# Performance work log

Hardware: AMD Instinct MI355X
Metric: run time of the kernel (lower is better)

The kernel has to match this reference:

```python
import jax, jax.numpy as jnp
import numpy as np
import math

DIM = 1024
HEADS = 16
HEAD_DIM = DIM // HEADS
FFN = 4096
B, S = 2, 2048
EPS = 1e-12


def layernorm(x, w, b):
    u = jnp.mean(x, axis=-1, keepdims=True)
    s = jnp.mean((x - u) ** 2, axis=-1, keepdims=True)
    return w * ((x - u) / jnp.sqrt(s + EPS)) + b


def setup_inputs() -> dict:
    key = jax.random.key(0)
    ks = jax.random.split(key, 8)
    scale = 0.02
    return {
        "x": jax.random.normal(ks[0], (B, S, DIM), dtype=jnp.float32),
        "mask": jnp.zeros((1, 1, S, S), dtype=jnp.float32),
        "wq": jax.random.normal(ks[1], (DIM, DIM), dtype=jnp.float32) * scale,
        "wk": jax.random.normal(ks[2], (DIM, DIM), dtype=jnp.float32) * scale,
        "wv": jax.random.normal(ks[3], (DIM, DIM), dtype=jnp.float32) * scale,
        "wo": jax.random.normal(ks[4], (DIM, DIM), dtype=jnp.float32) * scale,
        "w1": jax.random.normal(ks[5], (DIM, FFN), dtype=jnp.float32) * scale,
        "w2": jax.random.normal(ks[6], (FFN, DIM), dtype=jnp.float32) * scale,
        "ln1_w": jnp.ones((DIM,), dtype=jnp.float32),
        "ln1_b": jnp.zeros((DIM,), dtype=jnp.float32),
        "ln2_w": jnp.ones((DIM,), dtype=jnp.float32),
        "ln2_b": jnp.zeros((DIM,), dtype=jnp.float32),
    }


def reference(x, mask, wq, wk, wv, wo, w1, w2, ln1_w, ln1_b, ln2_w, ln2_b):
    # --- attention sub-block (pre-LN) ---
    h = layernorm(x, ln1_w, ln1_b)
    q = (h @ wq).reshape(B, S, HEADS, HEAD_DIM).transpose(0, 2, 1, 3)  # [B,H,S,D]
    k = (h @ wk).reshape(B, S, HEADS, HEAD_DIM).transpose(0, 2, 1, 3)
    v = (h @ wv).reshape(B, S, HEADS, HEAD_DIM).transpose(0, 2, 1, 3)
    scores = jnp.einsum("bhsd,bhtd->bhst", q, k) / math.sqrt(HEAD_DIM)
    scores = scores + mask
    probs = jax.nn.softmax(scores.astype(jnp.float32), axis=-1).astype(q.dtype)
    attn = jnp.einsum("bhst,bhtd->bhsd", probs, v)  # [B,H,S,D]
    attn = attn.transpose(0, 2, 1, 3).reshape(B, S, DIM)
    x = x + attn @ wo
    # --- FFN sub-block (pre-LN) ---
    h = layernorm(x, ln2_w, ln2_b)
    m = jax.nn.gelu(h @ w1, approximate=False) @ w2
    return x + m
```

## Files before the change

### kernel.cpp

```cpp
#include <hip/hip_runtime.h>
#include <math.h>


#define DIMSZ 1024
#define SEQ   2048
#define BATCH 2
#define NHEAD 16
#define HD    64
#define FFNSZ 4096
#define ROWS  (BATCH*SEQ)

typedef __attribute__((ext_vector_type(8))) short bf8_t;
typedef __attribute__((ext_vector_type(4))) float f4_t;

__device__ __forceinline__ unsigned short f2bf(float f) {
  union { float f; unsigned u; } c; c.f = f;
  unsigned u = c.u;
  return (unsigned short)((u + 0x7fffu + ((u >> 16) & 1u)) >> 16);
}

__device__ __forceinline__ float fast_exp2(float x) {
#if __has_builtin(__builtin_amdgcn_exp2f)
  return __builtin_amdgcn_exp2f(x);
#else
  return exp2f(x);
#endif
}

__device__ __forceinline__ unsigned int pk_trunc_bf16(float a, float b) {
#if __has_builtin(__builtin_amdgcn_perm)
  return __builtin_amdgcn_perm(__float_as_uint(b), __float_as_uint(a), 0x07060302u);
#else
  return (__float_as_uint(b) & 0xffff0000u) | (__float_as_uint(a) >> 16);
#endif
}

__device__ __forceinline__ void async16(const void* g, void* l) {
  __builtin_amdgcn_global_load_lds((const __attribute__((address_space(1))) void*)g,
                                   (__attribute__((address_space(3))) void*)l,
                                   16, 0, 0);
}

__device__ __forceinline__ f4_t mfma_bf16(bf8_t a, bf8_t b, f4_t c) {
  return __builtin_amdgcn_mfma_f32_16x16x32_bf16(a, b, c, 0, 0, 0);
}

__global__ __launch_bounds__(256) void ln_kernel(const float* __restrict__ x,
                                                 const float* __restrict__ w,
                                                 const float* __restrict__ b,
                                                 unsigned short* __restrict__ out) {
  int row  = blockIdx.x * 4 + (threadIdx.x >> 6);
  int lane = threadIdx.x & 63;
  const float4* xr = (const float4*)(x + (size_t)row * DIMSZ);
  float4 v[4];
  float s = 0.f, s2 = 0.f;
#pragma unroll
  for (int i = 0; i < 4; ++i) {
    v[i] = xr[lane + 64*i];
    s  += (v[i].x + v[i].y) + (v[i].z + v[i].w);
    s2 += (v[i].x*v[i].x + v[i].y*v[i].y) + (v[i].z*v[i].z + v[i].w*v[i].w);
  }
#pragma unroll
  for (int off = 32; off; off >>= 1) {
    s  += __shfl_xor(s,  off);
    s2 += __shfl_xor(s2, off);
  }
  float mean = s * (1.f/DIMSZ);
  float var  = s2 * (1.f/DIMSZ) - mean*mean;
  float rstd = rsqrtf(var + 1e-12f);
  const float4* wr = (const float4*)w;
  const float4* br = (const float4*)b;
#pragma unroll
  for (int i = 0; i < 4; ++i) {
    float4 wv = wr[lane + 64*i];
    float4 bv = br[lane + 64*i];
    ushort4 o;
    o.x = f2bf((v[i].x - mean) * rstd * wv.x + bv.x);
    o.y = f2bf((v[i].y - mean) * rstd * wv.y + bv.y);
    o.z = f2bf((v[i].z - mean) * rstd * wv.z + bv.z);
    o.w = f2bf((v[i].w - mean) * rstd * wv.w + bv.w);
    *(ushort4*)(out + (size_t)row * DIMSZ + (size_t)(lane + 64*i) * 4) = o;
  }
}

__global__ __launch_bounds__(256) void wtrans_kernel(const float* __restrict__ w,
                                                     unsigned short* __restrict__ wT,
                                                     int K, int N) {
  __shared__ float t[32][33];
  int tx = threadIdx.x & 31, ty = threadIdx.x >> 5;
  int n0 = blockIdx.x * 32, k0 = blockIdx.y * 32;
#pragma unroll
  for (int i = 0; i < 4; ++i)
    t[ty + 8*i][tx] = w[(size_t)(k0 + ty + 8*i) * N + n0 + tx];
  __syncthreads();
#pragma unroll
  for (int i = 0; i < 4; ++i)
    wT[(size_t)(n0 + ty + 8*i) * K + k0 + tx] = f2bf(t[tx][ty + 8*i]);
}

__global__ __launch_bounds__(256) void vt_kernel(const unsigned short* __restrict__ qkv,
                                                 unsigned short* __restrict__ vt) {
  __shared__ unsigned short tile[64][65];
  int bh = blockIdx.y, b = bh >> 4, h = bh & 15;
  int s0 = blockIdx.x * 64;
  int tx = threadIdx.x & 63, ty = threadIdx.x >> 6;
#pragma unroll
  for (int i = 0; i < 16; ++i) {
    int s = ty + i*4;
    tile[s][tx] = qkv[((size_t)(b*SEQ) + s0 + s) * 3072 + 2048 + h*HD + tx];
  }
  __syncthreads();
#pragma unroll
  for (int i = 0; i < 16; ++i) {
    int d = ty + i*4;
    vt[((size_t)bh * HD + d) * SEQ + s0 + tx] = tile[tx][d];
  }
}

template<int EPI>
__global__ __launch_bounds__(256) void gemm_bt(const unsigned short* __restrict__ A,
                                               const unsigned short* __restrict__ Bt,
                                               void* __restrict__ Cv,
                                               const float* __restrict__ res,
                                               int M, int N, int K) {
  __shared__ unsigned short As[128*32];
  __shared__ unsigned short Bs[128*32];
  int tid  = threadIdx.x;
  int wv   = tid >> 6, lane = tid & 63, quad = lane >> 4, ml = lane & 15;
  int wrow = (wv >> 1) * 64, wcol = (wv & 1) * 64;
  const unsigned short* Ab = A  + (size_t)blockIdx.y * 128 * K;
  const unsigned short* Bb = Bt + (size_t)blockIdx.x * 128 * K;

  f4_t acc[4][4];
#pragma unroll
  for (int i = 0; i < 4; ++i)
#pragma unroll
    for (int j = 0; j < 4; ++j) acc[i][j] = (f4_t){0.f, 0.f, 0.f, 0.f};

  int r0 = tid >> 2, c0 = (tid & 3) * 8;

  for (int k0 = 0; k0 < K; k0 += 32) {
    async16(Ab + (size_t)r0 * K + k0 + c0,        &As[(size_t)tid * 8]);
    async16(Ab + (size_t)(r0+64) * K + k0 + c0,   &As[((size_t)tid + 256) * 8]);
    async16(Bb + (size_t)r0 * K + k0 + c0,        &Bs[(size_t)tid * 8]);
    async16(Bb + (size_t)(r0+64) * K + k0 + c0,   &Bs[((size_t)tid + 256) * 8]);
    __syncthreads();

    bf8_t af[4], bfr[4];
#pragma unroll
    for (int i = 0; i < 4; ++i)
      af[i] = *(const bf8_t*)(&As[(wrow + i*16 + ml) * 32 + quad * 8]);
#pragma unroll
    for (int j = 0; j < 4; ++j)
      bfr[j] = *(const bf8_t*)(&Bs[(wcol + j*16 + ml) * 32 + quad * 8]);
#pragma unroll
    for (int i = 0; i < 4; ++i)
#pragma unroll
      for (int j = 0; j < 4; ++j)
        acc[i][j] = mfma_bf16(af[i], bfr[j], acc[i][j]);
    __syncthreads();
  }

#pragma unroll
  for (int i = 0; i < 4; ++i) {
    int grow = blockIdx.y * 128 + wrow + i*16 + quad*4;
#pragma unroll
    for (int j = 0; j < 4; ++j) {
      int gcol = blockIdx.x * 128 + wcol + j*16 + ml;
#pragma unroll
      for (int r = 0; r < 4; ++r) {
        size_t off = (size_t)(grow + r) * N + gcol;
        float v = acc[i][j][r];
        if constexpr (EPI == 2) {
          ((float*)Cv)[off] = res[off] + v;
        } else {
          if constexpr (EPI == 1)
            v = 0.5f * v * (1.f + erff(v * 0.70710678118654752f));
          ((unsigned short*)Cv)[off] = f2bf(v);
        }
      }
    }
  }
}

__global__ __launch_bounds__(256) void attn_kernel(const unsigned short* __restrict__ qkv,
                                                   const unsigned short* __restrict__ vt,
                                                   const float* __restrict__ mask,
                                                   unsigned short* __restrict__ attnout) {
  __shared__ unsigned short Ks[2][64][32];
  __shared__ unsigned short Vs[2][64][32];
  __shared__ unsigned short Ps[4][16][72];

  int bh = blockIdx.y, b = bh >> 4, h = bh & 15;
  int tid = threadIdx.x;
  int wv = tid >> 6, lane = tid & 63;
  int quad = lane >> 4, ml = lane & 15;
  int q0 = blockIdx.x * 64;
  int q  = q0 + wv * 16 + ml;

  const unsigned short* qrow = qkv + ((size_t)(b*SEQ) + q) * 3072 + h*HD;
  bf8_t qf0 = *(const bf8_t*)(qrow + quad*8);
  bf8_t qf1 = *(const bf8_t*)(qrow + 32 + quad*8);

  const unsigned short* kbase = qkv + (size_t)(b*SEQ) * 3072 + DIMSZ + h*HD;
  const unsigned short* vbase = vt + (size_t)bh * HD * SEQ;
  const float* mrow = mask + (size_t)q * SEQ;

  int srow = tid >> 2;
  int scol = (tid & 3) * 8;

  f4_t O[4];
#pragma unroll
  for (int dt = 0; dt < 4; ++dt) O[dt] = (f4_t){0.f, 0.f, 0.f, 0.f};
  float lR = 0.f;

  const float C1 = 0.18033688011112042f;
  const float C2 = 1.4426950408889634f;

  for (int t0 = 0; t0 < SEQ; t0 += 64) {
    float4 mv[4];
#pragma unroll
    for (int mt = 0; mt < 4; ++mt)
      mv[mt] = *(const float4*)(mrow + t0 + mt*16 + quad*4);

    __syncthreads();
#pragma unroll
    for (int dh = 0; dh < 2; ++dh)
      async16(kbase + (size_t)(t0 + srow) * 3072 + dh*32 + scol,
              &Ks[dh][0][0] + (size_t)tid * 8);
#pragma unroll
    for (int kc = 0; kc < 2; ++kc)
      async16(vbase + (size_t)srow * SEQ + t0 + kc*32 + scol,
              &Vs[kc][0][0] + (size_t)tid * 8);
    __syncthreads();

#pragma unroll
    for (int mt = 0; mt < 4; ++mt) {
      bf8_t kf0 = *(const bf8_t*)(&Ks[0][mt*16 + ml][quad*8]);
      bf8_t kf1 = *(const bf8_t*)(&Ks[1][mt*16 + ml][quad*8]);
      f4_t s = (f4_t){0.f, 0.f, 0.f, 0.f};
      s = mfma_bf16(kf0, qf0, s);
      s = mfma_bf16(kf1, qf1, s);
      float p0 = fast_exp2(fmaf(s[0], C1, mv[mt].x * C2));
      float p1 = fast_exp2(fmaf(s[1], C1, mv[mt].y * C2));
      float p2 = fast_exp2(fmaf(s[2], C1, mv[mt].z * C2));
      float p3 = fast_exp2(fmaf(s[3], C1, mv[mt].w * C2));
      lR += (p0 + p1) + (p2 + p3);
      unsigned int u01 = pk_trunc_bf16(p0, p1);
      unsigned int u23 = pk_trunc_bf16(p2, p3);
      uint2 pk; pk.x = u01; pk.y = u23;
      *(uint2*)(&Ps[wv][ml][mt*16 + quad*4]) = pk;
    }

#pragma unroll
    for (int kc = 0; kc < 2; ++kc) {
      bf8_t pf = *(const bf8_t*)(&Ps[wv][ml][kc*32 + quad*8]);
#pragma unroll
      for (int dt = 0; dt < 4; ++dt) {
        bf8_t vf = *(const bf8_t*)(&Vs[kc][dt*16 + ml][quad*8]);
        O[dt] = mfma_bf16(vf, pf, O[dt]);
      }
    }
  }

  lR += __shfl_xor(lR, 16);
  lR += __shfl_xor(lR, 32);
  float linv = 1.f / lR;
#pragma unroll
  for (int dt = 0; dt < 4; ++dt) {
    ushort4 o;
    o.x = f2bf(O[dt][0] * linv);
    o.y = f2bf(O[dt][1] * linv);
    o.z = f2bf(O[dt][2] * linv);
    o.w = f2bf(O[dt][3] * linv);
    *(ushort4*)(attnout + ((size_t)(b*SEQ) + q) * DIMSZ + h*HD + dt*16 + quad*4) = o;
  }
}

extern "C" void kernel_launch(void* const* d_in, const int* in_sizes, int n_in,
                              void* d_out, int out_size, void* d_ws, size_t ws_size,
                              hipStream_t stream) {
  const float* x    = (const float*)d_in[0];
  const float* mask = (const float*)d_in[1];
  const float* wq   = (const float*)d_in[2];
  const float* wk   = (const float*)d_in[3];
  const float* wvp  = (const float*)d_in[4];
  const float* wo   = (const float*)d_in[5];
  const float* w1   = (const float*)d_in[6];
  const float* w2   = (const float*)d_in[7];
  const float* ln1w = (const float*)d_in[8];
  const float* ln1b = (const float*)d_in[9];
  const float* ln2w = (const float*)d_in[10];
  const float* ln2b = (const float*)d_in[11];
  float* out = (float*)d_out;

  char* ws = (char*)d_ws;
  unsigned short* wqkvT  = (unsigned short*)(ws + 0);
  unsigned short* woT    = (unsigned short*)(ws + 6291456);
  unsigned short* w1T    = (unsigned short*)(ws + 8388608);
  unsigned short* w2T    = (unsigned short*)(ws + 16777216);
  unsigned short* attno  = (unsigned short*)(ws + 25165824);
  float*          x2     = (float*)         (ws + 33554432);
  unsigned short* hbuf   = (unsigned short*)(ws + 50331648);
  unsigned short* qkvb   = (unsigned short*)(ws + 58720256);
  unsigned short* vtb    = (unsigned short*)(ws + 83886080);
  unsigned short* gbuf   = (unsigned short*)(ws + 58720256);

  ln_kernel<<<ROWS/4, 256, 0, stream>>>(x, ln1w, ln1b, hbuf);
  wtrans_kernel<<<dim3(32, 32),  256, 0, stream>>>(wq,  wqkvT,                 1024, 1024);
  wtrans_kernel<<<dim3(32, 32),  256, 0, stream>>>(wk,  wqkvT + 1024*1024,     1024, 1024);
  wtrans_kernel<<<dim3(32, 32),  256, 0, stream>>>(wvp, wqkvT + 2*1024*1024,   1024, 1024);
  wtrans_kernel<<<dim3(32, 32),  256, 0, stream>>>(wo,  woT,                   1024, 1024);
  wtrans_kernel<<<dim3(128, 32), 256, 0, stream>>>(w1,  w1T,                   1024, 4096);
  wtrans_kernel<<<dim3(32, 128), 256, 0, stream>>>(w2,  w2T,                   4096, 1024);
  gemm_bt<0><<<dim3(3072/128, 4096/128), 256, 0, stream>>>(hbuf, wqkvT, qkvb, nullptr, ROWS, 3072, 1024);
  vt_kernel<<<dim3(SEQ/64, BATCH*NHEAD), 256, 0, stream>>>(qkvb, vtb);
  attn_kernel<<<dim3(SEQ/64, BATCH*NHEAD), 256, 0, stream>>>(qkvb, vtb, mask, attno);
  gemm_bt<2><<<dim3(1024/128, 4096/128), 256, 0, stream>>>(attno, woT, x2, x, ROWS, 1024, 1024);
  ln_kernel<<<ROWS/4, 256, 0, stream>>>(x2, ln2w, ln2b, hbuf);
  gemm_bt<1><<<dim3(4096/128, 4096/128), 256, 0, stream>>>(hbuf, w1T, gbuf, nullptr, ROWS, FFNSZ, 1024);
  gemm_bt<2><<<dim3(1024/128, 4096/128), 256, 0, stream>>>(gbuf, w2T, out, x2, ROWS, 1024, 4096);

  (void)in_sizes; (void)n_in; (void)out_size; (void)ws_size;
}
```

Baseline: 475.8 us.

## Double-buffer K/V tiles in attention and merge square weight transposes

The attention kernel now keeps two LDS buffers for K and V tiles and prefetches the next 64-key tile (plus its mask values) while computing the current one, removing the load-then-compute serialization per iteration. The four 1024x1024 weight transposes are merged into one launch using blockIdx.z to select the matrix, reducing launch count. This doubles the K/V shared memory per block and increases register use for the extra mask vectors, which could reduce occupancy.

After: 477.6 us. About the same (+0.4%).

```diff
diff --git a/kernel.cpp b/kernel.cpp
--- a/kernel.cpp
+++ b/kernel.cpp
@@ -81,6 +81,29 @@
     o.w = f2bf((v[i].w - mean) * rstd * wv.w + bv.w);
     *(ushort4*)(out + (size_t)row * DIMSZ + (size_t)(lane + 64*i) * 4) = o;
   }
+}
+
+__global__ __launch_bounds__(256) void wtrans4_kernel(const float* __restrict__ w0,
+                                                      const float* __restrict__ w1,
+                                                      const float* __restrict__ w2,
+                                                      const float* __restrict__ w3,
+                                                      unsigned short* __restrict__ o0,
+                                                      unsigned short* __restrict__ o1,
+                                                      unsigned short* __restrict__ o2,
+                                                      unsigned short* __restrict__ o3) {
+  const int K = 1024, N = 1024;
+  const float* w = (blockIdx.z == 0) ? w0 : (blockIdx.z == 1) ? w1 : (blockIdx.z == 2) ? w2 : w3;
+  unsigned short* wT = (blockIdx.z == 0) ? o0 : (blockIdx.z == 1) ? o1 : (blockIdx.z == 2) ? o2 : o3;
+  __shared__ float t[32][33];
+  int tx = threadIdx.x & 31, ty = threadIdx.x >> 5;
+  int n0 = blockIdx.x * 32, k0 = blockIdx.y * 32;
+#pragma unroll
+  for (int i = 0; i < 4; ++i)
+    t[ty + 8*i][tx] = w[(size_t)(k0 + ty + 8*i) * N + n0 + tx];
+  __syncthreads();
+#pragma unroll
+  for (int i = 0; i < 4; ++i)
+    wT[(size_t)(n0 + ty + 8*i) * K + k0 + tx] = f2bf(t[tx][ty + 8*i]);
 }
 
 __global__ __launch_bounds__(256) void wtrans_kernel(const float* __restrict__ w,
@@ -187,8 +210,8 @@
                                                    const unsigned short* __restrict__ vt,
                                                    const float* __restrict__ mask,
                                                    unsigned short* __restrict__ attnout) {
-  __shared__ unsigned short Ks[2][64][32];
-  __shared__ unsigned short Vs[2][64][32];
+  __shared__ unsigned short Ks[2][2][64][32];
+  __shared__ unsigned short Vs[2][2][64][32];
   __shared__ unsigned short Ps[4][16][72];
 
   int bh = blockIdx.y, b = bh >> 4, h = bh & 15;
@@ -217,27 +240,26 @@
   const float C1 = 0.18033688011112042f;
   const float C2 = 1.4426950408889634f;
 
-  for (int t0 = 0; t0 < SEQ; t0 += 64) {
-    float4 mv[4];
+  auto stage = [&](int t0, int buf) {
+#pragma unroll
+    for (int dh = 0; dh < 2; ++dh)
+      async16(kbase + (size_t)(t0 + srow) * 3072 + dh*32 + scol,
+              &Ks[buf][dh][0][0] + (size_t)tid * 8);
+#pragma unroll
+    for (int kc = 0; kc < 2; ++kc)
+      async16(vbase + (size_t)srow * SEQ + t0 + kc*32 + scol,
+              &Vs[buf][kc][0][0] + (size_t)tid * 8);
+  };
+  auto loadmask = [&](int t0, float4* mv) {
 #pragma unroll
     for (int mt = 0; mt < 4; ++mt)
       mv[mt] = *(const float4*)(mrow + t0 + mt*16 + quad*4);
-
-    __syncthreads();
-#pragma unroll
-    for (int dh = 0; dh < 2; ++dh)
-      async16(kbase + (size_t)(t0 + srow) * 3072 + dh*32 + scol,
-              &Ks[dh][0][0] + (size_t)tid * 8);
-#pragma unroll
-    for (int kc = 0; kc < 2; ++kc)
-      async16(vbase + (size_t)srow * SEQ + t0 + kc*32 + scol,
-              &Vs[kc][0][0] + (size_t)tid * 8);
-    __syncthreads();
-
+  };
+  auto compute = [&](int buf, const float4* mv) {
 #pragma unroll
     for (int mt = 0; mt < 4; ++mt) {
-      bf8_t kf0 = *(const bf8_t*)(&Ks[0][mt*16 + ml][quad*8]);
-      bf8_t kf1 = *(const bf8_t*)(&Ks[1][mt*16 + ml][quad*8]);
+      bf8_t kf0 = *(const bf8_t*)(&Ks[buf][0][mt*16 + ml][quad*8]);
+      bf8_t kf1 = *(const bf8_t*)(&Ks[buf][1][mt*16 + ml][quad*8]);
       f4_t s = (f4_t){0.f, 0.f, 0.f, 0.f};
       s = mfma_bf16(kf0, qf0, s);
       s = mfma_bf16(kf1, qf1, s);
@@ -246,21 +268,38 @@
       float p2 = fast_exp2(fmaf(s[2], C1, mv[mt].z * C2));
       float p3 = fast_exp2(fmaf(s[3], C1, mv[mt].w * C2));
       lR += (p0 + p1) + (p2 + p3);
-      unsigned int u01 = pk_trunc_bf16(p0, p1);
-      unsigned int u23 = pk_trunc_bf16(p2, p3);
-      uint2 pk; pk.x = u01; pk.y = u23;
+      uint2 pk;
+      pk.x = pk_trunc_bf16(p0, p1);
+      pk.y = pk_trunc_bf16(p2, p3);
       *(uint2*)(&Ps[wv][ml][mt*16 + quad*4]) = pk;
     }
-
 #pragma unroll
     for (int kc = 0; kc < 2; ++kc) {
       bf8_t pf = *(const bf8_t*)(&Ps[wv][ml][kc*32 + quad*8]);
 #pragma unroll
       for (int dt = 0; dt < 4; ++dt) {
-        bf8_t vf = *(const bf8_t*)(&Vs[kc][dt*16 + ml][quad*8]);
+        bf8_t vf = *(const bf8_t*)(&Vs[buf][kc][dt*16 + ml][quad*8]);
         O[dt] = mfma_bf16(vf, pf, O[dt]);
       }
     }
+  };
+
+  float4 mcur[4], mnxt[4];
+  stage(0, 0);
+  loadmask(0, mcur);
+
+#pragma unroll 1
+  for (int c = 0; c < SEQ/64; c += 2) {
+    __syncthreads();
+    loadmask((c+1)*64, mnxt);
+    stage((c+1)*64, 1);
+    compute(0, mcur);
+    __syncthreads();
+    if (c + 2 < SEQ/64) {
+      loadmask((c+2)*64, mcur);
+      stage((c+2)*64, 0);
+    }
+    compute(1, mnxt);
   }
 
   lR += __shfl_xor(lR, 16);
@@ -307,12 +346,10 @@
   unsigned short* gbuf   = (unsigned short*)(ws + 58720256);
 
   ln_kernel<<<ROWS/4, 256, 0, stream>>>(x, ln1w, ln1b, hbuf);
-  wtrans_kernel<<<dim3(32, 32),  256, 0, stream>>>(wq,  wqkvT,                 1024, 1024);
-  wtrans_kernel<<<dim3(32, 32),  256, 0, stream>>>(wk,  wqkvT + 1024*1024,     1024, 1024);
-  wtrans_kernel<<<dim3(32, 32),  256, 0, stream>>>(wvp, wqkvT + 2*1024*1024,   1024, 1024);
-  wtrans_kernel<<<dim3(32, 32),  256, 0, stream>>>(wo,  woT,                   1024, 1024);
-  wtrans_kernel<<<dim3(128, 32), 256, 0, stream>>>(w1,  w1T,                   1024, 4096);
-  wtrans_kernel<<<dim3(32, 128), 256, 0, stream>>>(w2,  w2T,                   4096, 1024);
+  wtrans4_kernel<<<dim3(32, 32, 4), 256, 0, stream>>>(wq, wk, wvp, wo,
+      wqkvT, wqkvT + 1024*1024, wqkvT + 2*1024*1024, woT);
+  wtrans_kernel<<<dim3(128, 32), 256, 0, stream>>>(w1, w1T, 1024, 4096);
+  wtrans_kernel<<<dim3(32, 128), 256, 0, stream>>>(w2, w2T, 4096, 1024);
   gemm_bt<0><<<dim3(3072/128, 4096/128), 256, 0, stream>>>(hbuf, wqkvT, qkvb, nullptr, ROWS, 3072, 1024);
   vt_kernel<<<dim3(SEQ/64, BATCH*NHEAD), 256, 0, stream>>>(qkvb, vtb);
   attn_kernel<<<dim3(SEQ/64, BATCH*NHEAD), 256, 0, stream>>>(qkvb, vtb, mask, attno);
```
